# Kernel tuning notes

Hardware: AMD Instinct MI355X
Metric: run time of the kernel (lower is better)

Reference implementation:

```python
import jax, jax.numpy as jnp
import numpy as np

HEADS = 8
WH, WW = 8, 8
DIM = 256
B = 4096
N = WH * WW  # 64


def _rel_index():
    ch, cw = np.meshgrid(np.arange(WH), np.arange(WW), indexing='ij')
    coords = np.stack([ch.ravel(), cw.ravel()])  # (2, N)
    rel = coords[:, :, None] - coords[:, None, :]  # (2, N, N)
    rel = rel.transpose(1, 2, 0)
    rel[:, :, 0] += WH - 1
    rel[:, :, 1] += WW - 1
    rel[:, :, 0] *= 2 * WW - 1
    return jnp.asarray(rel.sum(-1), dtype=jnp.int32)  # (N, N)


def setup_inputs() -> dict:
    key = jax.random.key(0)
    ks = jax.random.split(key, 6)
    x = jax.random.normal(ks[0], (B, N, DIM), dtype=jnp.float32)
    attn_mask = jnp.zeros((1, HEADS, N, N), dtype=jnp.float32)
    w_qkv = jax.random.normal(ks[1], (3 * DIM, DIM), dtype=jnp.float32) * 0.02
    w_proj = jax.random.normal(ks[2], (DIM, DIM), dtype=jnp.float32) * 0.02
    b_proj = jax.random.normal(ks[3], (DIM,), dtype=jnp.float32) * 0.02
    table = jax.random.normal(ks[4], (225, HEADS), dtype=jnp.float32) * 0.02
    return {"x": x, "attn_mask": attn_mask, "w_qkv": w_qkv, "w_proj": w_proj,
            "b_proj": b_proj, "table": table, "rel_index": _rel_index()}


def reference(x, attn_mask, w_qkv, w_proj, b_proj, table, rel_index):
    Bn, Nn, C = x.shape
    hd = C // HEADS
    qkv = (x @ w_qkv.T).reshape(Bn, Nn, 3, HEADS, hd)
    q = qkv[:, :, 0].transpose(0, 2, 1, 3)  # (B,h,N,d)
    k = qkv[:, :, 1].transpose(0, 2, 1, 3)
    v = qkv[:, :, 2].transpose(0, 2, 1, 3)
    scale = 1.0 / jnp.sqrt(jnp.asarray(hd, dtype=x.dtype))
    attn = jnp.einsum('bhnd,bhmd->bhnm', q, k) * scale
    bias = table[rel_index]  # (N,N,h)
    attn = attn + bias.transpose(2, 0, 1)[None] + attn_mask
    attn = jax.nn.softmax(attn, axis=-1)
    out = jnp.einsum('bhnm,bhmd->bhnd', attn, v)
    out = out.transpose(0, 2, 1, 3).reshape(Bn, Nn, C)
    return out @ w_proj.T + b_proj
```

## Files before the change

kernel.cpp:

```cpp
#include <hip/hip_runtime.h>
#include <hip/hip_bf16.h>

#define HEADS 8
#define NTOK 64
#define DIM 256
#define HD 32

typedef __attribute__((ext_vector_type(8))) short bf16x8;
typedef __attribute__((ext_vector_type(4))) float f32x4;
typedef unsigned short u16;

__device__ __forceinline__ u16 f2bf(float f) {
    union { float f; unsigned u; } c; c.f = f;
    unsigned u = c.u;
    unsigned rounded = u + 0x7FFF + ((u >> 16) & 1);
    return (u16)(rounded >> 16);
}

__global__ void prep_kernel(const float* __restrict__ wqkv,
                            const float* __restrict__ wproj,
                            const float* __restrict__ table,
                            const int* __restrict__ rel_index,
                            const float* __restrict__ mask,
                            u16* __restrict__ wq_bf,
                            u16* __restrict__ wp_bf,
                            float* __restrict__ bias) {
    const int NQ = 768 * 256;
    const int NP = 256 * 256;
    const int NB = HEADS * NTOK * NTOK;
    int total = NQ + NP + NB;
    for (int i = blockIdx.x * blockDim.x + threadIdx.x; i < total;
         i += gridDim.x * blockDim.x) {
        if (i < NQ) {
            wq_bf[i] = f2bf(wqkv[i]);
        } else if (i < NQ + NP) {
            wp_bf[i - NQ] = f2bf(wproj[i - NQ]);
        } else {
            int j = i - (NQ + NP);
            int h = j >> 12;
            int nm = j & 4095;
            bias[j] = table[rel_index[nm] * HEADS + h] + mask[j];
        }
    }
}

__launch_bounds__(512, 2)
__global__ void win_attn_kernel(const float* __restrict__ x,
                                const u16* __restrict__ wq_bf,
                                const u16* __restrict__ wp_bf,
                                const float* __restrict__ bias,
                                const float* __restrict__ b_proj,
                                float* __restrict__ out) {
    __shared__ u16 s_xb[64 * 264];
    __shared__ u16 s_q[64 * 264];
    __shared__ u16 s_k[64 * 264];
    __shared__ u16 s_vt[256 * 72];

    const int b = blockIdx.x;
    const int tid = threadIdx.x;
    const int w = tid >> 6;
    const int l = tid & 63;
    const int l16 = l & 15;
    const int lhi = l >> 4;

    const float* xw = x + (size_t)b * (NTOK * DIM);
#pragma unroll
    for (int it = 0; it < 8; ++it) {
        int idx4 = tid + it * 512;
        float4 v = reinterpret_cast<const float4*>(xw)[idx4];
        int row = idx4 >> 6;
        int col = (idx4 & 63) * 4;
        ushort4 o;
        o.x = f2bf(v.x); o.y = f2bf(v.y); o.z = f2bf(v.z); o.w = f2bf(v.w);
        *reinterpret_cast<ushort4*>(&s_xb[row * 264 + col]) = o;
    }
    __syncthreads();

    f32x4 acc[6][4];
    const f32x4 zero = {0.f, 0.f, 0.f, 0.f};
#pragma unroll
    for (int t = 0; t < 6; ++t)
#pragma unroll
        for (int rt = 0; rt < 4; ++rt) acc[t][rt] = zero;

    for (int ks = 0; ks < 8; ++ks) {
        const int k0 = ks * 32 + lhi * 8;
        bf16x8 afrag[4];
#pragma unroll
        for (int rt = 0; rt < 4; ++rt)
            afrag[rt] = *reinterpret_cast<const bf16x8*>(&s_xb[(rt * 16 + l16) * 264 + k0]);
#pragma unroll
        for (int t = 0; t < 6; ++t) {
            int o = (w + 8 * t) * 16 + l16;
            bf16x8 bfrag = *reinterpret_cast<const bf16x8*>(&wq_bf[o * 256 + k0]);
#pragma unroll
            for (int rt = 0; rt < 4; ++rt)
                acc[t][rt] = __builtin_amdgcn_mfma_f32_16x16x32_bf16(afrag[rt], bfrag, acc[t][rt], 0, 0, 0);
        }
    }
#pragma unroll
    for (int t = 0; t < 6; ++t) {
        int o = (w + 8 * t) * 16 + l16;
        int which = o >> 8;
        int rem = o & 255;
#pragma unroll
        for (int rt = 0; rt < 4; ++rt) {
#pragma unroll
            for (int r = 0; r < 4; ++r) {
                int row = rt * 16 + lhi * 4 + r;
                u16 v = f2bf(acc[t][rt][r]);
                if (which == 0)      s_q[row * 264 + rem] = v;
                else if (which == 1) s_k[row * 264 + rem] = v;
                else                 s_vt[rem * 72 + row] = v;
            }
        }
    }
    __syncthreads();

    {
        const int h = w;
        u16* Psub = &s_xb[w * 1152];
        bf16x8 vfrag[2][2], qf[4], kf[4];
#pragma unroll
        for (int dt = 0; dt < 2; ++dt)
#pragma unroll
            for (int kv = 0; kv < 2; ++kv)
                vfrag[dt][kv] = *reinterpret_cast<const bf16x8*>(
                    &s_vt[(h * 32 + dt * 16 + l16) * 72 + kv * 32 + lhi * 8]);
#pragma unroll
        for (int rt = 0; rt < 4; ++rt)
            qf[rt] = *reinterpret_cast<const bf16x8*>(&s_q[(rt * 16 + l16) * 264 + h * 32 + lhi * 8]);
#pragma unroll
        for (int ct = 0; ct < 4; ++ct)
            kf[ct] = *reinterpret_cast<const bf16x8*>(&s_k[(ct * 16 + l16) * 264 + h * 32 + lhi * 8]);

        f32x4 sacc[4][4];
#pragma unroll
        for (int rt = 0; rt < 4; ++rt)
#pragma unroll
            for (int ct = 0; ct < 4; ++ct)
                sacc[rt][ct] = __builtin_amdgcn_mfma_f32_16x16x32_bf16(qf[rt], kf[ct], zero, 0, 0, 0);

        const float scale = 0.17677669529663687f;
        const float* biash = bias + h * 4096;
#pragma unroll
        for (int rt = 0; rt < 4; ++rt) {
            float p[4][4];
#pragma unroll
            for (int r = 0; r < 4; ++r) {
                int row = rt * 16 + lhi * 4 + r;
                float m = -1e30f;
#pragma unroll
                for (int ct = 0; ct < 4; ++ct) {
                    float s = sacc[rt][ct][r] * scale + biash[row * 64 + ct * 16 + l16];
                    p[r][ct] = s;
                    m = fmaxf(m, s);
                }
#pragma unroll
                for (int msk = 1; msk <= 8; msk <<= 1)
                    m = fmaxf(m, __shfl_xor(m, msk, 64));
                float sum = 0.f;
#pragma unroll
                for (int ct = 0; ct < 4; ++ct) {
                    p[r][ct] = __expf(p[r][ct] - m);
                    sum += p[r][ct];
                }
#pragma unroll
                for (int msk = 1; msk <= 8; msk <<= 1)
                    sum += __shfl_xor(sum, msk, 64);
                float inv = 1.0f / sum;
#pragma unroll
                for (int ct = 0; ct < 4; ++ct)
                    Psub[(lhi * 4 + r) * 72 + ct * 16 + l16] = f2bf(p[r][ct] * inv);
            }
            bf16x8 pa0 = *reinterpret_cast<const bf16x8*>(&Psub[l16 * 72 + lhi * 8]);
            bf16x8 pa1 = *reinterpret_cast<const bf16x8*>(&Psub[l16 * 72 + 32 + lhi * 8]);
            f32x4 oacc[2];
#pragma unroll
            for (int dt = 0; dt < 2; ++dt) {
                oacc[dt] = __builtin_amdgcn_mfma_f32_16x16x32_bf16(pa0, vfrag[dt][0], zero, 0, 0, 0);
                oacc[dt] = __builtin_amdgcn_mfma_f32_16x16x32_bf16(pa1, vfrag[dt][1], oacc[dt], 0, 0, 0);
            }
#pragma unroll
            for (int dt = 0; dt < 2; ++dt)
#pragma unroll
                for (int r = 0; r < 4; ++r) {
                    int row = rt * 16 + lhi * 4 + r;
                    s_k[row * 264 + h * 32 + dt * 16 + l16] = f2bf(oacc[dt][r]);
                }
        }
    }
    __syncthreads();

    f32x4 pacc[2][4];
#pragma unroll
    for (int t = 0; t < 2; ++t)
#pragma unroll
        for (int rt = 0; rt < 4; ++rt) pacc[t][rt] = zero;

    for (int ks = 0; ks < 8; ++ks) {
        const int k0 = ks * 32 + lhi * 8;
        bf16x8 afrag[4];
#pragma unroll
        for (int rt = 0; rt < 4; ++rt)
            afrag[rt] = *reinterpret_cast<const bf16x8*>(&s_k[(rt * 16 + l16) * 264 + k0]);
#pragma unroll
        for (int t = 0; t < 2; ++t) {
            int o = (w + 8 * t) * 16 + l16;
            bf16x8 bfrag = *reinterpret_cast<const bf16x8*>(&wp_bf[o * 256 + k0]);
#pragma unroll
            for (int rt = 0; rt < 4; ++rt)
                pacc[t][rt] = __builtin_amdgcn_mfma_f32_16x16x32_bf16(afrag[rt], bfrag, pacc[t][rt], 0, 0, 0);
        }
    }
    float* outw = out + (size_t)b * (NTOK * DIM);
#pragma unroll
    for (int t = 0; t < 2; ++t) {
        int col = (w + 8 * t) * 16 + l16;
        float bp = b_proj[col];
#pragma unroll
        for (int rt = 0; rt < 4; ++rt)
#pragma unroll
            for (int r = 0; r < 4; ++r) {
                int row = rt * 16 + lhi * 4 + r;
                outw[row * 256 + col] = pacc[t][rt][r] + bp;
            }
    }
}

extern "C" void kernel_launch(void* const* d_in, const int* in_sizes, int n_in,
                              void* d_out, int out_size, void* d_ws, size_t ws_size,
                              hipStream_t stream) {
    const float* x     = (const float*)d_in[0];
    const float* mask  = (const float*)d_in[1];
    const float* wqkv  = (const float*)d_in[2];
    const float* wproj = (const float*)d_in[3];
    const float* bproj = (const float*)d_in[4];
    const float* table = (const float*)d_in[5];
    const int*   relix = (const int*)d_in[6];

    u16*   wq_bf = (u16*)d_ws;
    u16*   wp_bf = wq_bf + 768 * 256;
    float* bias  = (float*)(wp_bf + 256 * 256);

    prep_kernel<<<64, 512, 0, stream>>>(wqkv, wproj, table, relix, mask,
                                        wq_bf, wp_bf, bias);
    win_attn_kernel<<<4096, 512, 0, stream>>>(x, wq_bf, wp_bf, bias, bproj,
                                              (float*)d_out);
}
```

Measured before the change: 442.6 us.

## Use 1024-thread blocks with 16 waves splitting QKV, attention and projection work

Doubles the workgroup to 16 waves. Each wave now computes a third of the QKV output tiles, half the query row tiles of one head, and one projection column tile. Shared memory is merged into one buffer, and the P scratch tiles are placed over the x buffer after an extra barrier, with a 68-element row stride. The aim is fewer accumulators per wave (lower register pressure) and more waves in flight to hide latency. The cost is an extra block-wide sync, and launch bounds that ask the compiler to fit more waves per CU.

```diff
diff --git a/kernel.cpp b/kernel.cpp
--- a/kernel.cpp
+++ b/kernel.cpp
@@ -4,7 +4,6 @@
 #define HEADS 8
 #define NTOK 64
 #define DIM 256
-#define HD 32
 
 typedef __attribute__((ext_vector_type(8))) short bf16x8;
 typedef __attribute__((ext_vector_type(4))) float f32x4;
@@ -44,17 +43,18 @@
     }
 }
 
-__launch_bounds__(512, 2)
+__launch_bounds__(1024, 4)
 __global__ void win_attn_kernel(const float* __restrict__ x,
                                 const u16* __restrict__ wq_bf,
                                 const u16* __restrict__ wp_bf,
                                 const float* __restrict__ bias,
                                 const float* __restrict__ b_proj,
                                 float* __restrict__ out) {
-    __shared__ u16 s_xb[64 * 264];
-    __shared__ u16 s_q[64 * 264];
-    __shared__ u16 s_k[64 * 264];
-    __shared__ u16 s_vt[256 * 72];
+    __shared__ u16 smem[69120];
+    u16* s_x  = smem;
+    u16* s_q  = smem + 16896;
+    u16* s_k  = smem + 33792;
+    u16* s_vt = smem + 50688;
 
     const int b = blockIdx.x;
     const int tid = threadIdx.x;
@@ -65,21 +65,21 @@
 
     const float* xw = x + (size_t)b * (NTOK * DIM);
 #pragma unroll
-    for (int it = 0; it < 8; ++it) {
-        int idx4 = tid + it * 512;
+    for (int it = 0; it < 4; ++it) {
+        int idx4 = tid + it * 1024;
         float4 v = reinterpret_cast<const float4*>(xw)[idx4];
         int row = idx4 >> 6;
         int col = (idx4 & 63) * 4;
         ushort4 o;
         o.x = f2bf(v.x); o.y = f2bf(v.y); o.z = f2bf(v.z); o.w = f2bf(v.w);
-        *reinterpret_cast<ushort4*>(&s_xb[row * 264 + col]) = o;
+        *reinterpret_cast<ushort4*>(&s_x[row * 264 + col]) = o;
     }
     __syncthreads();
 
-    f32x4 acc[6][4];
+    f32x4 acc[3][4];
     const f32x4 zero = {0.f, 0.f, 0.f, 0.f};
 #pragma unroll
-    for (int t = 0; t < 6; ++t)
+    for (int t = 0; t < 3; ++t)
 #pragma unroll
         for (int rt = 0; rt < 4; ++rt) acc[t][rt] = zero;
 
@@ -88,39 +88,39 @@
         bf16x8 afrag[4];
 #pragma unroll
         for (int rt = 0; rt < 4; ++rt)
-            afrag[rt] = *reinterpret_cast<const bf16x8*>(&s_xb[(rt * 16 + l16) * 264 + k0]);
-#pragma unroll
-        for (int t = 0; t < 6; ++t) {
-            int o = (w + 8 * t) * 16 + l16;
+            afrag[rt] = *reinterpret_cast<const bf16x8*>(&s_x[(rt * 16 + l16) * 264 + k0]);
+#pragma unroll
+        for (int t = 0; t < 3; ++t) {
+            int o = (w + 16 * t) * 16 + l16;
             bf16x8 bfrag = *reinterpret_cast<const bf16x8*>(&wq_bf[o * 256 + k0]);
 #pragma unroll
             for (int rt = 0; rt < 4; ++rt)
                 acc[t][rt] = __builtin_amdgcn_mfma_f32_16x16x32_bf16(afrag[rt], bfrag, acc[t][rt], 0, 0, 0);
         }
     }
-#pragma unroll
-    for (int t = 0; t < 6; ++t) {
-        int o = (w + 8 * t) * 16 + l16;
-        int which = o >> 8;
-        int rem = o & 255;
-#pragma unroll
-        for (int rt = 0; rt < 4; ++rt) {
-#pragma unroll
-            for (int r = 0; r < 4; ++r) {
-                int row = rt * 16 + lhi * 4 + r;
-                u16 v = f2bf(acc[t][rt][r]);
-                if (which == 0)      s_q[row * 264 + rem] = v;
-                else if (which == 1) s_k[row * 264 + rem] = v;
-                else                 s_vt[rem * 72 + row] = v;
+    {
+        const int rem = w * 16 + l16;
+#pragma unroll
+        for (int t = 0; t < 3; ++t) {
+#pragma unroll
+            for (int rt = 0; rt < 4; ++rt) {
+#pragma unroll
+                for (int r = 0; r < 4; ++r) {
+                    int row = rt * 16 + lhi * 4 + r;
+                    u16 v = f2bf(acc[t][rt][r]);
+                    if (t == 0)      s_q[row * 264 + rem] = v;
+                    else if (t == 1) s_k[row * 264 + rem] = v;
+                    else             s_vt[rem * 72 + row] = v;
+                }
             }
         }
     }
     __syncthreads();
 
     {
-        const int h = w;
-        u16* Psub = &s_xb[w * 1152];
-        bf16x8 vfrag[2][2], qf[4], kf[4];
+        const int h = w >> 1;
+        const int half = w & 1;
+        bf16x8 vfrag[2][2], qf[2], kf[4];
 #pragma unroll
         for (int dt = 0; dt < 2; ++dt)
 #pragma unroll
@@ -128,32 +128,36 @@
                 vfrag[dt][kv] = *reinterpret_cast<const bf16x8*>(
                     &s_vt[(h * 32 + dt * 16 + l16) * 72 + kv * 32 + lhi * 8]);
 #pragma unroll
-        for (int rt = 0; rt < 4; ++rt)
-            qf[rt] = *reinterpret_cast<const bf16x8*>(&s_q[(rt * 16 + l16) * 264 + h * 32 + lhi * 8]);
+        for (int i = 0; i < 2; ++i) {
+            int rt = half * 2 + i;
+            qf[i] = *reinterpret_cast<const bf16x8*>(&s_q[(rt * 16 + l16) * 264 + h * 32 + lhi * 8]);
+        }
 #pragma unroll
         for (int ct = 0; ct < 4; ++ct)
             kf[ct] = *reinterpret_cast<const bf16x8*>(&s_k[(ct * 16 + l16) * 264 + h * 32 + lhi * 8]);
-
-        f32x4 sacc[4][4];
-#pragma unroll
-        for (int rt = 0; rt < 4; ++rt)
-#pragma unroll
-            for (int ct = 0; ct < 4; ++ct)
-                sacc[rt][ct] = __builtin_amdgcn_mfma_f32_16x16x32_bf16(qf[rt], kf[ct], zero, 0, 0, 0);
-
+        __syncthreads();
+
+        u16* Pw = smem + w * 1088;
         const float scale = 0.17677669529663687f;
         const float* biash = bias + h * 4096;
-#pragma unroll
-        for (int rt = 0; rt < 4; ++rt) {
-            float p[4][4];
+
+#pragma unroll
+        for (int i = 0; i < 2; ++i) {
+            const int rt = half * 2 + i;
+            f32x4 sacc[4];
+#pragma unroll
+            for (int ct = 0; ct < 4; ++ct)
+                sacc[ct] = __builtin_amdgcn_mfma_f32_16x16x32_bf16(qf[i], kf[ct], zero, 0, 0, 0);
+
 #pragma unroll
             for (int r = 0; r < 4; ++r) {
                 int row = rt * 16 + lhi * 4 + r;
+                float p[4];
                 float m = -1e30f;
 #pragma unroll
                 for (int ct = 0; ct < 4; ++ct) {
-                    float s = sacc[rt][ct][r] * scale + biash[row * 64 + ct * 16 + l16];
-                    p[r][ct] = s;
+                    float s = sacc[ct][r] * scale + biash[row * 64 + ct * 16 + l16];
+                    p[ct] = s;
                     m = fmaxf(m, s);
                 }
 #pragma unroll
@@ -162,8 +166,8 @@
                 float sum = 0.f;
 #pragma unroll
                 for (int ct = 0; ct < 4; ++ct) {
-                    p[r][ct] = __expf(p[r][ct] - m);
-                    sum += p[r][ct];
+                    p[ct] = __expf(p[ct] - m);
+                    sum += p[ct];
                 }
 #pragma unroll
                 for (int msk = 1; msk <= 8; msk <<= 1)
@@ -171,10 +175,10 @@
                 float inv = 1.0f / sum;
 #pragma unroll
                 for (int ct = 0; ct < 4; ++ct)
-                    Psub[(lhi * 4 + r) * 72 + ct * 16 + l16] = f2bf(p[r][ct] * inv);
-            }
-            bf16x8 pa0 = *reinterpret_cast<const bf16x8*>(&Psub[l16 * 72 + lhi * 8]);
-            bf16x8 pa1 = *reinterpret_cast<const bf16x8*>(&Psub[l16 * 72 + 32 + lhi * 8]);
+                    Pw[(lhi * 4 + r) * 68 + ct * 16 + l16] = f2bf(p[ct] * inv);
+            }
+            bf16x8 pa0 = *reinterpret_cast<const bf16x8*>(&Pw[l16 * 68 + lhi * 8]);
+            bf16x8 pa1 = *reinterpret_cast<const bf16x8*>(&Pw[l16 * 68 + 32 + lhi * 8]);
             f32x4 oacc[2];
 #pragma unroll
             for (int dt = 0; dt < 2; ++dt) {
@@ -192,11 +196,9 @@
     }
     __syncthreads();
 
-    f32x4 pacc[2][4];
-#pragma unroll
-    for (int t = 0; t < 2; ++t)
-#pragma unroll
-        for (int rt = 0; rt < 4; ++rt) pacc[t][rt] = zero;
+    f32x4 pacc[4];
+#pragma unroll
+    for (int rt = 0; rt < 4; ++rt) pacc[rt] = zero;
 
     for (int ks = 0; ks < 8; ++ks) {
         const int k0 = ks * 32 + lhi * 8;
@@ -204,26 +206,21 @@
 #pragma unroll
         for (int rt = 0; rt < 4; ++rt)
             afrag[rt] = *reinterpret_cast<const bf16x8*>(&s_k[(rt * 16 + l16) * 264 + k0]);
-#pragma unroll
-        for (int t = 0; t < 2; ++t) {
-            int o = (w + 8 * t) * 16 + l16;
-            bf16x8 bfrag = *reinterpret_cast<const bf16x8*>(&wp_bf[o * 256 + k0]);
-#pragma unroll
-            for (int rt = 0; rt < 4; ++rt)
-                pacc[t][rt] = __builtin_amdgcn_mfma_f32_16x16x32_bf16(afrag[rt], bfrag, pacc[t][rt], 0, 0, 0);
-        }
+        bf16x8 bfrag = *reinterpret_cast<const bf16x8*>(&wp_bf[(w * 16 + l16) * 256 + k0]);
+#pragma unroll
+        for (int rt = 0; rt < 4; ++rt)
+            pacc[rt] = __builtin_amdgcn_mfma_f32_16x16x32_bf16(afrag[rt], bfrag, pacc[rt], 0, 0, 0);
     }
     float* outw = out + (size_t)b * (NTOK * DIM);
-#pragma unroll
-    for (int t = 0; t < 2; ++t) {
-        int col = (w + 8 * t) * 16 + l16;
+    {
+        int col = w * 16 + l16;
         float bp = b_proj[col];
 #pragma unroll
         for (int rt = 0; rt < 4; ++rt)
 #pragma unroll
             for (int r = 0; r < 4; ++r) {
                 int row = rt * 16 + lhi * 4 + r;
-                outw[row * 256 + col] = pacc[t][rt][r] + bp;
+                outw[row * 256 + col] = pacc[rt][r] + bp;
             }
     }
 }
@@ -245,6 +242,6 @@
 
     prep_kernel<<<64, 512, 0, stream>>>(wqkv, wproj, table, relix, mask,
                                         wq_bf, wp_bf, bias);
-    win_attn_kernel<<<4096, 512, 0, stream>>>(x, wq_bf, wp_bf, bias, bproj,
-                                              (float*)d_out);
-}
+    win_attn_kernel<<<4096, 1024, 0, stream>>>(x, wq_bf, wp_bf, bias, bproj,
+                                               (float*)d_out);
+}
```

Result: no change. 435.8 us (-1.5%).
